# Kernel optimization log

Hardware: AMD Instinct MI355X
Metric: run time of the kernel (lower is better)

The kernel has to match this reference:

```python
import jax, jax.numpy as jnp
import numpy as np

B, S, E, H = 1, 2048, 1024, 16
D = E // H  # head_dim = 64


def setup_inputs() -> dict:
    key = jax.random.key(0)
    ks = jax.random.split(key, 9)
    sd = 0.02
    hidden_states = jax.random.normal(ks[0], (B, S, E), dtype=jnp.float32)
    # causal mask: positions with mask==0 are filled with -inf (per masked_fill_)
    mask = jnp.tril(jnp.ones((1, 1, S, S), dtype=bool))
    Wq = jax.random.normal(ks[1], (E, E), dtype=jnp.float32) * sd
    bq = jax.random.normal(ks[2], (E,), dtype=jnp.float32) * sd
    Wk = jax.random.normal(ks[3], (D, E), dtype=jnp.float32) * sd
    bk = jax.random.normal(ks[4], (D,), dtype=jnp.float32) * sd
    Wv = jax.random.normal(ks[5], (D, E), dtype=jnp.float32) * sd
    bv = jax.random.normal(ks[6], (D,), dtype=jnp.float32) * sd
    Wo = jax.random.normal(ks[7], (E, E), dtype=jnp.float32) * sd
    bo = jax.random.normal(ks[8], (E,), dtype=jnp.float32) * sd
    return {"hidden_states": hidden_states, "mask": mask,
            "Wq": Wq, "bq": bq, "Wk": Wk, "bk": bk,
            "Wv": Wv, "bv": bv, "Wo": Wo, "bo": bo}


def reference(hidden_states, mask, Wq, bq, Wk, bk, Wv, bv, Wo, bo):
    bsz, tgt_len, embed_dim = hidden_states.shape
    # projections (torch Linear: x @ W^T + b)
    q = hidden_states @ Wq.T + bq                       # [B, S, E]
    q = q.reshape(bsz, tgt_len, H, D).transpose(0, 2, 1, 3)  # [B, H, S, D]
    k = hidden_states @ Wk.T + bk                       # [B, S, D] shared single KV head
    v = hidden_states @ Wv.T + bv                       # [B, S, D]
    scaling = jnp.sqrt(jnp.asarray(D, dtype=hidden_states.dtype))
    # QK^T with implicit broadcast of the shared K head (instead of expand)
    scores = jnp.einsum('bhqd,bkd->bhqk', q, k) / scaling   # [B, H, S, S]
    scores = jnp.where(mask, scores, -jnp.inf)
    probs = jax.nn.softmax(scores, axis=-1)             # dropout p=0 -> identity
    attn = jnp.einsum('bhqk,bkd->bhqd', probs, v)       # [B, H, S, D]
    attn = attn.transpose(0, 2, 1, 3).reshape(bsz, tgt_len, H * D)
    return attn @ Wo.T + bo                             # [B, S, E]
```

## Files before the change

kernel.cpp:

```cpp
#include <hip/hip_runtime.h>
#include <hip/hip_bf16.h>

typedef __hip_bfloat16 bf16;
typedef __attribute__((ext_vector_type(8))) short short8;
typedef __attribute__((ext_vector_type(4))) short short4v;
typedef __attribute__((ext_vector_type(4))) float f32x4;

__device__ __forceinline__ short8 ld8(const void* p) { return *(const short8*)p; }
__device__ __forceinline__ short4v ld4(const void* p) { return *(const short4v*)p; }

__device__ __forceinline__ void async_cp16(bf16* lds, const bf16* g) {
    __builtin_amdgcn_global_load_lds(
        (const __attribute__((address_space(1))) unsigned int*)g,
        (__attribute__((address_space(3))) unsigned int*)lds, 16, 0, 0);
}

struct bf4 { bf16 a, b, c, d; };

__global__ void cast_kernel(const float* __restrict__ s0, bf16* __restrict__ d0, int n0_,
                            const float* __restrict__ s1, bf16* __restrict__ d1, int n1_,
                            const float* __restrict__ s2, bf16* __restrict__ d2, int n2_,
                            const float* __restrict__ s3, bf16* __restrict__ d3, int n3_,
                            const float* __restrict__ s4, bf16* __restrict__ d4, int n4_) {
    const float* srcs[5] = {s0, s1, s2, s3, s4};
    bf16* dsts[5] = {d0, d1, d2, d3, d4};
    int ns[5] = {n0_, n1_, n2_, n3_, n4_};
    int stride = gridDim.x * blockDim.x;
    int t0 = blockIdx.x * blockDim.x + threadIdx.x;
#pragma unroll
    for (int a = 0; a < 5; ++a) {
        const float4* src = (const float4*)srcs[a];
        bf4* dst = (bf4*)dsts[a];
        int n4 = ns[a] >> 2;
        for (int i = t0; i < n4; i += stride) {
            float4 v = src[i];
            bf4 o = {__float2bfloat16(v.x), __float2bfloat16(v.y),
                     __float2bfloat16(v.z), __float2bfloat16(v.w)};
            dst[i] = o;
        }
    }
}

#define GEMM_STAGE(dst, src_base, row0, ldk)                                   \
    _Pragma("unroll")                                                          \
    for (int u = 0; u < 4; ++u) {                                              \
        int t = wave * 4 + u;                                                  \
        int row = t * 4 + (lane >> 4);                                         \
        int gsrc = (lane & 15) ^ (row & 15);                                   \
        async_cp16(&dst[t * 4][0], src_base + (size_t)(row0 + row) * ldk + k0 + gsrc * 8); \
    }

__global__ void qkv_proj_kernel(const bf16* __restrict__ A,
                                const bf16* __restrict__ Wq, const bf16* __restrict__ Wk,
                                const bf16* __restrict__ Wv,
                                const float* __restrict__ bq, const float* __restrict__ bk,
                                const float* __restrict__ bv,
                                bf16* __restrict__ qo, bf16* __restrict__ ko,
                                bf16* __restrict__ vto, int M, int K) {
    __shared__ __align__(16) bf16 As[64][128];
    __shared__ __align__(16) bf16 Bs[64][128];

    const int lin = blockIdx.x;
    const int w = (lin & 7) * 72 + (lin >> 3);
    const int nt = w % 18;
    const int m0 = (w / 18) * 64;

    const bf16* W;
    const float* bias;
    int mode, nw0;
    if (nt < 16)      { W = Wq; bias = bq; mode = 0; nw0 = nt * 64; }
    else if (nt == 16){ W = Wk; bias = bk; mode = 1; nw0 = 0; }
    else              { W = Wv; bias = bv; mode = 2; nw0 = 0; }

    const int tid = threadIdx.x;
    const int wave = tid >> 6, lane = tid & 63;
    const int l16 = lane & 15, quad = lane >> 4;
    const int wr = wave >> 1, wc = wave & 1;

    f32x4 acc[2][2];
    const f32x4 z = {0.f, 0.f, 0.f, 0.f};
#pragma unroll
    for (int mi = 0; mi < 2; ++mi)
#pragma unroll
        for (int ni = 0; ni < 2; ++ni) acc[mi][ni] = z;

    for (int k0 = 0; k0 < K; k0 += 128) {
        GEMM_STAGE(As, A, m0, K)
        GEMM_STAGE(Bs, W, nw0, K)
        __syncthreads();

        short8 af[2][4], bfr[2][4];
#pragma unroll
        for (int mi = 0; mi < 2; ++mi) {
            int R = wr * 32 + mi * 16 + l16;
#pragma unroll
            for (int kc = 0; kc < 4; ++kc)
                af[mi][kc] = ld8(&As[R][((kc * 4 + quad) ^ (R & 15)) * 8]);
        }
#pragma unroll
        for (int ni = 0; ni < 2; ++ni) {
            int r = wc * 32 + ni * 16 + l16;
#pragma unroll
            for (int kc = 0; kc < 4; ++kc)
                bfr[ni][kc] = ld8(&Bs[r][((kc * 4 + quad) ^ (r & 15)) * 8]);
        }
#pragma unroll
        for (int kc = 0; kc < 4; ++kc)
#pragma unroll
            for (int mi = 0; mi < 2; ++mi)
#pragma unroll
                for (int ni = 0; ni < 2; ++ni)
                    acc[mi][ni] = __builtin_amdgcn_mfma_f32_16x16x32_bf16(
                        af[mi][kc], bfr[ni][kc], acc[mi][ni], 0, 0, 0);
        __syncthreads();
    }

#pragma unroll
    for (int mi = 0; mi < 2; ++mi)
#pragma unroll
        for (int ni = 0; ni < 2; ++ni)
#pragma unroll
            for (int r = 0; r < 4; ++r) {
                int row = m0 + wr * 32 + mi * 16 + quad * 4 + r;
                int c = wc * 32 + ni * 16 + l16;
                float v = acc[mi][ni][r] + bias[nw0 + c];
                if (mode == 0)
                    qo[(size_t)row * 1024 + nt * 64 + c] = __float2bfloat16(v * 0.125f);
                else if (mode == 1)
                    ko[(size_t)row * 64 + c] = __float2bfloat16(v);
                else
                    vto[(size_t)c * M + row] = __float2bfloat16(v);
            }
}

__global__ void gemm_bt_mfma(const bf16* __restrict__ A, const bf16* __restrict__ W,
                             const float* __restrict__ bias, float* __restrict__ C,
                             int M, int N, int K) {
    __shared__ __align__(16) bf16 As[64][128];
    __shared__ __align__(16) bf16 Bs[64][128];
    const int tid = threadIdx.x;
    const int wave = tid >> 6, lane = tid & 63;
    const int l16 = lane & 15, quad = lane >> 4;
    const int wr = wave >> 1, wc = wave & 1;

    const int ntn = N / 64;
    const int tot = (M / 64) * ntn;
    const int cpx = tot >> 3;
    const int lin = blockIdx.x;
    const int w = (lin & 7) * cpx + (lin >> 3);
    const int n0 = (w % ntn) * 64;
    const int m0 = (w / ntn) * 64;

    f32x4 acc[2][2];
    const f32x4 z = {0.f, 0.f, 0.f, 0.f};
#pragma unroll
    for (int mi = 0; mi < 2; ++mi)
#pragma unroll
        for (int ni = 0; ni < 2; ++ni) acc[mi][ni] = z;

    for (int k0 = 0; k0 < K; k0 += 128) {
        GEMM_STAGE(As, A, m0, K)
        GEMM_STAGE(Bs, W, n0, K)
        __syncthreads();

        short8 af[2][4], bfr[2][4];
#pragma unroll
        for (int mi = 0; mi < 2; ++mi) {
            int R = wr * 32 + mi * 16 + l16;
#pragma unroll
            for (int kc = 0; kc < 4; ++kc)
                af[mi][kc] = ld8(&As[R][((kc * 4 + quad) ^ (R & 15)) * 8]);
        }
#pragma unroll
        for (int ni = 0; ni < 2; ++ni) {
            int r = wc * 32 + ni * 16 + l16;
#pragma unroll
            for (int kc = 0; kc < 4; ++kc)
                bfr[ni][kc] = ld8(&Bs[r][((kc * 4 + quad) ^ (r & 15)) * 8]);
        }
#pragma unroll
        for (int kc = 0; kc < 4; ++kc)
#pragma unroll
            for (int mi = 0; mi < 2; ++mi)
#pragma unroll
                for (int ni = 0; ni < 2; ++ni)
                    acc[mi][ni] = __builtin_amdgcn_mfma_f32_16x16x32_bf16(
                        af[mi][kc], bfr[ni][kc], acc[mi][ni], 0, 0, 0);
        __syncthreads();
    }

#pragma unroll
    for (int mi = 0; mi < 2; ++mi)
#pragma unroll
        for (int ni = 0; ni < 2; ++ni)
#pragma unroll
            for (int r = 0; r < 4; ++r) {
                int row = m0 + wr * 32 + mi * 16 + quad * 4 + r;
                int col = n0 + wc * 32 + ni * 16 + l16;
                C[(size_t)row * N + col] = acc[mi][ni][r] + bias[col];
            }
}

__global__ void flash_mfma_kernel(const bf16* __restrict__ Q, const bf16* __restrict__ Kg,
                                  const bf16* __restrict__ VT,
                                  bf16* __restrict__ Opart, float* __restrict__ Lpart,
                                  bf16* __restrict__ attn, int S) {
    const int s = blockIdx.x;
    int i, c;
    if (s < 32)      { c = 0; i = s; }
    else if (s < 56) { c = 1; i = s - 24; }
    else if (s < 72) { c = 2; i = s - 40; }
    else             { c = 3; i = s - 48; }

    __shared__ __align__(16) bf16 Ks[64][64];
    __shared__ __align__(16) bf16 Vt[64][64];

    const int h = blockIdx.y;
    const int q0 = i * 64;
    const int tid = threadIdx.x;
    const int wave = tid >> 6, lane = tid & 63;
    const int l16 = lane & 15, quad = lane >> 4;
    const int lr = lane >> 3, lsw = (lane & 7) ^ (lr & 7);
    const int qrow = q0 + wave * 16;

    short8 qf[2];
#pragma unroll
    for (int kc = 0; kc < 2; ++kc)
        qf[kc] = ld8(Q + (size_t)(qrow + l16) * 1024 + h * 64 + kc * 32 + quad * 8);

    f32x4 of[4];
    const f32x4 z = {0.f, 0.f, 0.f, 0.f};
#pragma unroll
    for (int dt = 0; dt < 4; ++dt) of[dt] = z;
    float lsum = 0.f;

    const int jt0 = c * 8;
    const int jt1 = min(c * 8 + 8, i + 1);

    for (int jt = jt0; jt < jt1; ++jt) {
        const int j0 = jt * 64;
#pragma unroll
        for (int u = 0; u < 2; ++u) {
            int t = wave * 2 + u;
            async_cp16(&Ks[t * 8][0], Kg + (size_t)(j0 + t * 8 + lr) * 64 + lsw * 8);
            async_cp16(&Vt[t * 8][0], VT + (size_t)(t * 8 + lr) * S + j0 + lsw * 8);
        }
        __syncthreads();

        f32x4 sc[4];
#pragma unroll
        for (int nt = 0; nt < 4; ++nt) {
            int R = nt * 16 + l16;
            sc[nt] = __builtin_amdgcn_mfma_f32_16x16x32_bf16(
                ld8(&Ks[R][(quad ^ (R & 7)) * 8]), qf[0], z, 0, 0, 0);
            sc[nt] = __builtin_amdgcn_mfma_f32_16x16x32_bf16(
                ld8(&Ks[R][((4 + quad) ^ (R & 7)) * 8]), qf[1], sc[nt], 0, 0, 0);
        }
        if (j0 + 63 > qrow) {
#pragma unroll
            for (int nt = 0; nt < 4; ++nt)
#pragma unroll
                for (int r = 0; r < 4; ++r)
                    if (j0 + nt * 16 + quad * 4 + r > qrow + l16) sc[nt][r] = -1e30f;
        }

        short4v p4[4];
#pragma unroll
        for (int nt = 0; nt < 4; ++nt)
#pragma unroll
            for (int r = 0; r < 4; ++r) {
                bf16 b = __float2bfloat16(__expf(sc[nt][r]));
                lsum += __bfloat162float(b);
                p4[nt][r] = *reinterpret_cast<short*>(&b);
            }

#pragma unroll
        for (int dt = 0; dt < 4; ++dt) {
            int d = dt * 16 + l16;
            int xr = d & 7;
#pragma unroll
            for (int nt = 0; nt < 4; ++nt) {
                int g = 2 * nt + (quad >> 1);
                short4v vf = ld4(&Vt[d][((g ^ xr) * 8) + (quad & 1) * 4]);
                of[dt] = __builtin_amdgcn_mfma_f32_16x16x16bf16_1k(
                    p4[nt], vf, of[dt], 0, 0, 0);
            }
        }
        __syncthreads();
    }

    float Lred = lsum;
    Lred += __shfl_xor(Lred, 16);
    Lred += __shfl_xor(Lred, 32);

    if (s < 8) {
        float inv[4];
#pragma unroll
        for (int r = 0; r < 4; ++r)
            inv[r] = 1.f / __shfl(Lred, quad * 4 + r);
#pragma unroll
        for (int dt = 0; dt < 4; ++dt)
#pragma unroll
            for (int r = 0; r < 4; ++r) {
                int row = q0 + wave * 16 + quad * 4 + r;
                attn[(size_t)row * 1024 + h * 64 + dt * 16 + l16] =
                    __float2bfloat16(of[dt][r] * inv[r]);
            }
        return;
    }

    bf16* Op = Opart + ((size_t)s * 16 + h) * 4096;
#pragma unroll
    for (int dt = 0; dt < 4; ++dt)
#pragma unroll
        for (int r = 0; r < 4; ++r) {
            int row = wave * 16 + quad * 4 + r;
            Op[row * 64 + dt * 16 + l16] = __float2bfloat16(of[dt][r]);
        }
    if (quad == 0) {
        float* L = Lpart + ((size_t)s * 16 + h) * 64;
        L[wave * 16 + l16] = Lred;
    }
}

__global__ void flash_merge_kernel(const bf16* __restrict__ Opart,
                                   const float* __restrict__ Lpart,
                                   bf16* __restrict__ attn) {
    const int i = blockIdx.x + 8, h = blockIdx.y;
    const int nch = (i >> 3) + 1;
    const int tid = threadIdx.x;
    const int row = tid >> 2, cg = (tid & 3) * 16;

    float L = 0.f;
    for (int cc = 0; cc < nch; ++cc) {
        int s = (cc == 0) ? i : (cc == 1) ? 24 + i : (cc == 2) ? 40 + i : 48 + i;
        L += Lpart[((size_t)s * 16 + h) * 64 + row];
    }
    float inv = 1.f / L;

    float o[16];
#pragma unroll
    for (int j = 0; j < 16; ++j) o[j] = 0.f;
    for (int cc = 0; cc < nch; ++cc) {
        int s = (cc == 0) ? i : (cc == 1) ? 24 + i : (cc == 2) ? 40 + i : 48 + i;
        const bf16* Op = Opart + ((size_t)s * 16 + h) * 4096 + row * 64 + cg;
#pragma unroll
        for (int j = 0; j < 16; ++j) o[j] += __bfloat162float(Op[j]);
    }
    bf16* dst = attn + (size_t)(i * 64 + row) * 1024 + h * 64 + cg;
#pragma unroll
    for (int j = 0; j < 16; ++j) dst[j] = __float2bfloat16(o[j] * inv);
}

extern "C" void kernel_launch(void* const* d_in, const int* in_sizes, int n_in,
                              void* d_out, int out_size, void* d_ws, size_t ws_size,
                              hipStream_t stream) {
    const int S = 2048, E = 1024, D = 64;

    const float* hs = (const float*)d_in[0];
    const float* Wq = (const float*)d_in[2];
    const float* bq = (const float*)d_in[3];
    const float* Wk = (const float*)d_in[4];
    const float* bk = (const float*)d_in[5];
    const float* Wv = (const float*)d_in[6];
    const float* bv = (const float*)d_in[7];
    const float* Wo = (const float*)d_in[8];
    const float* bo = (const float*)d_in[9];
    float* out = (float*)d_out;

    bf16* ws = (bf16*)d_ws;
    bf16* hsb = ws;
    bf16* wqb = hsb + (size_t)S * E;
    bf16* wkb = wqb + (size_t)E * E;
    bf16* wvb = wkb + (size_t)D * E;
    bf16* wob = wvb + (size_t)D * E;
    bf16* q = wob + (size_t)E * E;
    bf16* kbuf = q + (size_t)S * E;
    bf16* vt = kbuf + (size_t)S * D;
    bf16* attn = vt + (size_t)S * D;
    bf16* Opart = attn + (size_t)S * E;
    float* Lpart = (float*)(Opart + (size_t)1280 * 4096);

    cast_kernel<<<512, 256, 0, stream>>>(hs, hsb, S * E,
                                         Wq, wqb, E * E,
                                         Wk, wkb, D * E,
                                         Wv, wvb, D * E,
                                         Wo, wob, E * E);
    qkv_proj_kernel<<<dim3(18 * (S / 64)), 256, 0, stream>>>(hsb, wqb, wkb, wvb,
                                                             bq, bk, bv,
                                                             q, kbuf, vt, S, E);
    flash_mfma_kernel<<<dim3(80, 16), 256, 0, stream>>>(q, kbuf, vt, Opart, Lpart, attn, S);
    flash_merge_kernel<<<dim3(24, 16), 256, 0, stream>>>(Opart, Lpart, attn);
    gemm_bt_mfma<<<dim3((S / 64) * (E / 64)), 256, 0, stream>>>(attn, wob, bo, out, S, E, E);
}
```

Baseline: 134.5 us.

## Double-buffer K/V tiles in flash attention kernel with prefetch and setprio

```diff
diff --git a/kernel.cpp b/kernel.cpp
--- a/kernel.cpp
+++ b/kernel.cpp
@@ -212,8 +212,8 @@
     else if (s < 72) { c = 2; i = s - 40; }
     else             { c = 3; i = s - 48; }
 
-    __shared__ __align__(16) bf16 Ks[64][64];
-    __shared__ __align__(16) bf16 Vt[64][64];
+    __shared__ __align__(16) bf16 Ks[2][64][64];
+    __shared__ __align__(16) bf16 Vt[2][64][64];
 
     const int h = blockIdx.y;
     const int q0 = i * 64;
@@ -236,25 +236,39 @@
 
     const int jt0 = c * 8;
     const int jt1 = min(c * 8 + 8, i + 1);
-
-    for (int jt = jt0; jt < jt1; ++jt) {
+    const int nits = jt1 - jt0;
+
+#define STAGE_KV(buf, jt_)                                                       \
+    do {                                                                         \
+        const int j0_ = (jt_) * 64;                                              \
+        _Pragma("unroll")                                                        \
+        for (int u = 0; u < 2; ++u) {                                            \
+            int t = wave * 2 + u;                                                \
+            async_cp16(&Ks[buf][t * 8][0],                                       \
+                       Kg + (size_t)(j0_ + t * 8 + lr) * 64 + lsw * 8);          \
+            async_cp16(&Vt[buf][t * 8][0],                                       \
+                       VT + (size_t)(t * 8 + lr) * S + j0_ + lsw * 8);           \
+        }                                                                        \
+    } while (0)
+
+    STAGE_KV(0, jt0);
+    __syncthreads();
+
+    for (int it = 0; it < nits; ++it) {
+        const int jt = jt0 + it;
         const int j0 = jt * 64;
-#pragma unroll
-        for (int u = 0; u < 2; ++u) {
-            int t = wave * 2 + u;
-            async_cp16(&Ks[t * 8][0], Kg + (size_t)(j0 + t * 8 + lr) * 64 + lsw * 8);
-            async_cp16(&Vt[t * 8][0], VT + (size_t)(t * 8 + lr) * S + j0 + lsw * 8);
-        }
-        __syncthreads();
-
+        const int cur = it & 1;
+        if (it + 1 < nits) STAGE_KV(cur ^ 1, jt + 1);
+
+        __builtin_amdgcn_s_setprio(1);
         f32x4 sc[4];
 #pragma unroll
         for (int nt = 0; nt < 4; ++nt) {
             int R = nt * 16 + l16;
             sc[nt] = __builtin_amdgcn_mfma_f32_16x16x32_bf16(
-                ld8(&Ks[R][(quad ^ (R & 7)) * 8]), qf[0], z, 0, 0, 0);
+                ld8(&Ks[cur][R][(quad ^ (R & 7)) * 8]), qf[0], z, 0, 0, 0);
             sc[nt] = __builtin_amdgcn_mfma_f32_16x16x32_bf16(
-                ld8(&Ks[R][((4 + quad) ^ (R & 7)) * 8]), qf[1], sc[nt], 0, 0, 0);
+                ld8(&Ks[cur][R][((4 + quad) ^ (R & 7)) * 8]), qf[1], sc[nt], 0, 0, 0);
         }
         if (j0 + 63 > qrow) {
 #pragma unroll
@@ -281,13 +295,15 @@
 #pragma unroll
             for (int nt = 0; nt < 4; ++nt) {
                 int g = 2 * nt + (quad >> 1);
-                short4v vf = ld4(&Vt[d][((g ^ xr) * 8) + (quad & 1) * 4]);
+                short4v vf = ld4(&Vt[cur][d][((g ^ xr) * 8) + (quad & 1) * 4]);
                 of[dt] = __builtin_amdgcn_mfma_f32_16x16x16bf16_1k(
                     p4[nt], vf, of[dt], 0, 0, 0);
             }
         }
+        __builtin_amdgcn_s_setprio(0);
         __syncthreads();
     }
+#undef STAGE_KV
 
     float Lred = lsum;
     Lred += __shfl_xor(Lred, 16);
```

After: 140.2 us. 1.04x slower.
